# Performance work log

Measured on AMD Instinct MI355X. Metric: run time of the kernel, lower is better.

Reference implementation:

```python
import jax, jax.numpy as jnp
import numpy as np

EMBED_DIM = 1024
NUM_HEADS = 16
HEAD_DIM = EMBED_DIM // NUM_HEADS


def setup_inputs() -> dict:
    key = jax.random.key(0)
    ks = jax.random.split(key, 5)
    s = 0.02
    return {
        "x": jax.random.normal(ks[0], (2, 2048, EMBED_DIM), dtype=jnp.float32),
        "w_qkv": jax.random.normal(ks[1], (EMBED_DIM, 3 * EMBED_DIM), dtype=jnp.float32) * s,
        "b_qkv": jnp.zeros((3 * EMBED_DIM,), dtype=jnp.float32),
        "w_out": jax.random.normal(ks[2], (EMBED_DIM, EMBED_DIM), dtype=jnp.float32) * s,
        "b_out": jnp.zeros((EMBED_DIM,), dtype=jnp.float32),
    }


def reference(x, w_qkv, b_qkv, w_out, b_out):
    B, T, C = x.shape
    qkv = x @ w_qkv + b_qkv                       # [B,T,3C]
    q, k, v = jnp.split(qkv, 3, axis=-1)
    # [B,T,C] -> [B,H,T,Dh]
    def heads(t):
        return t.reshape(B, T, NUM_HEADS, HEAD_DIM).transpose(0, 2, 1, 3)
    q, k, v = heads(q), heads(k), heads(v)
    scale = 1.0 / np.sqrt(HEAD_DIM).astype(np.float32)
    scores = jnp.einsum("bhqd,bhkd->bhqk", q, k) * scale  # [B,H,T,T]
    causal = jnp.tril(jnp.ones((T, T), dtype=bool))
    scores = jnp.where(causal[None, None], scores, -jnp.inf)
    attn = jax.nn.softmax(scores, axis=-1)
    out = jnp.einsum("bhqk,bhkd->bhqd", attn, v)  # [B,H,T,Dh]
    out = out.transpose(0, 2, 1, 3).reshape(B, T, C)
    return out @ w_out + b_out
```

## Files before the change

### kernel.cpp

```cpp
#include <hip/hip_runtime.h>

typedef unsigned short u16;
typedef unsigned int u32;
typedef __attribute__((ext_vector_type(8))) short bf16x8;
typedef __attribute__((ext_vector_type(4))) float f32x4;
typedef __attribute__((ext_vector_type(16))) float f32x16;

#define TOK   4096
#define EMB   1024
#define NQKV  3072
#define TSEQ  2048
#define NH    16

__device__ __forceinline__ u16 f2b(float f) {
  union { float f; unsigned u; } v; v.f = f;
  unsigned r = v.u + 0x7FFFu + ((v.u >> 16) & 1u);
  return (u16)(r >> 16);
}

__device__ __forceinline__ u32 pack_rn(float a, float b) {
  u32 ua = __float_as_uint(a) + 0x8000u;
  u32 ub = __float_as_uint(b) + 0x8000u;
  return __builtin_amdgcn_perm(ub, ua, 0x07060302u);
}

__device__ __forceinline__ f32x16 zero16() {
  f32x16 z;
#pragma unroll
  for (int i = 0; i < 16; i++) z[i] = 0.f;
  return z;
}

__device__ __forceinline__ void gload16(const void* g, void* l) {
  __builtin_amdgcn_global_load_lds((const __attribute__((address_space(1))) void*)g,
                                   (__attribute__((address_space(3))) void*)l, 16, 0, 0);
}


__global__ __launch_bounds__(256) void prep_kernel(const float* __restrict__ x,
                                                   u16* __restrict__ x_bf,
                                                   const float* __restrict__ w_qkv,
                                                   u16* __restrict__ wqkvT,
                                                   const float* __restrict__ w_out,
                                                   u16* __restrict__ woutT) {
  __shared__ u16 sm[64][65];
  int bid = blockIdx.x, tid = threadIdx.x;
  if (bid < 4096) {
    int i = bid * 256 + tid;
    float4 v = ((const float4*)x)[i];
    union { u16 us[4]; uint2 u2; } o;
    o.us[0] = f2b(v.x); o.us[1] = f2b(v.y); o.us[2] = f2b(v.z); o.us[3] = f2b(v.w);
    ((uint2*)x_bf)[i] = o.u2;
    return;
  }
  const float* src; u16* dst; int R, C, bx, by;
  if (bid < 4096 + 768) {
    int t = bid - 4096; bx = t % 48; by = t / 48;
    src = w_qkv; dst = wqkvT; R = EMB; C = NQKV;
  } else {
    int t = bid - 4096 - 768; bx = t & 15; by = t >> 4;
    src = w_out; dst = woutT; R = EMB; C = EMB;
  }
  int c0 = bx * 64, r0 = by * 64;
#pragma unroll
  for (int i = 0; i < 16; i++) {
    int idx = tid + i * 256;
    int r = idx >> 6, c = idx & 63;
    sm[r][c] = f2b(src[(size_t)(r0 + r) * C + c0 + c]);
  }
  __syncthreads();
#pragma unroll
  for (int i = 0; i < 16; i++) {
    int idx = tid + i * 256;
    int cc = idx >> 6, rr = idx & 63;
    dst[(size_t)(c0 + cc) * R + r0 + rr] = sm[rr][cc];
  }
}

__global__ __launch_bounds__(256) void transpose_v(const u16* __restrict__ V,
                                                   u16* __restrict__ Vt) {
  __shared__ u16 sm[64][72];
  int t0 = blockIdx.x * 64, bh = blockIdx.y;
  size_t base = (size_t)bh * TSEQ * 64;
  int tid = threadIdx.x;
  int r = tid >> 2, c = (tid & 3) * 16;
  *(bf16x8*)&sm[r][c]     = *(const bf16x8*)&V[base + (size_t)(t0 + r) * 64 + c];
  *(bf16x8*)&sm[r][c + 8] = *(const bf16x8*)&V[base + (size_t)(t0 + r) * 64 + c + 8];
  __syncthreads();
  int d = tid >> 2, tc = (tid & 3) * 16;
  union { u16 us[16]; uint4 v4[2]; } o;
#pragma unroll
  for (int i = 0; i < 16; i++) o.us[i] = sm[tc + i][d];
  *(uint4*)&Vt[base + (size_t)d * TSEQ + t0 + tc]     = o.v4[0];
  *(uint4*)&Vt[base + (size_t)d * TSEQ + t0 + tc + 8] = o.v4[1];
}


template <int MODE, int TN>
__global__ __launch_bounds__(256) void gemm_bt(const u16* __restrict__ A,
                                               const u16* __restrict__ Bt,
                                               const float* __restrict__ bias,
                                               u16* __restrict__ qb, u16* __restrict__ kb,
                                               u16* __restrict__ vb, float* __restrict__ outp,
                                               int K, int N) {
  constexpr int CT = TN / 32;
  constexpr int RB = TN / 32;
  __shared__ u16 As[2][128][64];
  __shared__ u16 Bs[2][TN][64];
  int tid = threadIdx.x;
  int m0 = blockIdx.y * 128, n0 = blockIdx.x * TN;
  int lane = tid & 63, wid = tid >> 6;
  int wm = (wid >> 1) * 64;
  int wn = (wid & 1) * (TN / 2);
  int l15 = lane & 15, quad = lane >> 4;
  int srow = lane >> 3;
  int scol = (((lane & 7) ^ srow) * 8);

  f32x4 acc[4][CT];
#pragma unroll
  for (int i = 0; i < 4; i++)
#pragma unroll
    for (int j = 0; j < CT; j++) acc[i][j] = (f32x4){0.f, 0.f, 0.f, 0.f};

  const u16* Ag = A + (size_t)(m0 + wid * 32 + srow) * K + scol;
  const u16* Bg = Bt + (size_t)(n0 + wid * (TN / 4) + srow) * K + scol;

#pragma unroll
  for (int i = 0; i < 4; i++)
    gload16(Ag + (size_t)(i * 8) * K, &As[0][wid * 32 + i * 8][0]);
#pragma unroll
  for (int i = 0; i < RB; i++)
    gload16(Bg + (size_t)(i * 8) * K, &Bs[0][wid * (TN / 4) + i * 8][0]);
  __syncthreads();

  int cur = 0;
  for (int k0 = 0; k0 < K; k0 += 64) {
    if (k0 + 64 < K) {
      int kn = k0 + 64;
#pragma unroll
      for (int i = 0; i < 4; i++)
        gload16(Ag + (size_t)(i * 8) * K + kn, &As[cur ^ 1][wid * 32 + i * 8][0]);
#pragma unroll
      for (int i = 0; i < RB; i++)
        gload16(Bg + (size_t)(i * 8) * K + kn, &Bs[cur ^ 1][wid * (TN / 4) + i * 8][0]);
    }

#pragma unroll
    for (int ks = 0; ks < 2; ks++) {
      bf16x8 af[4], bfr[CT];
#pragma unroll
      for (int rt = 0; rt < 4; rt++)
        af[rt] = *(const bf16x8*)&As[cur][wm + rt * 16 + l15][((ks * 4 + quad) ^ (l15 & 7)) * 8];
#pragma unroll
      for (int ct = 0; ct < CT; ct++)
        bfr[ct] = *(const bf16x8*)&Bs[cur][wn + ct * 16 + l15][((ks * 4 + quad) ^ (l15 & 7)) * 8];
#pragma unroll
      for (int rt = 0; rt < 4; rt++)
#pragma unroll
        for (int ct = 0; ct < CT; ct++)
          acc[rt][ct] = __builtin_amdgcn_mfma_f32_16x16x32_bf16(bfr[ct], af[rt], acc[rt][ct], 0, 0, 0);
    }
    __syncthreads();
    cur ^= 1;
  }

#pragma unroll
  for (int rt = 0; rt < 4; rt++) {
#pragma unroll
    for (int ct = 0; ct < CT; ct++) {
      int m = m0 + wm + rt * 16 + l15;
      int nb = n0 + wn + ct * 16 + quad * 4;
      float4 b4 = *(const float4*)&bias[nb];
      float v0 = acc[rt][ct][0] + b4.x, v1 = acc[rt][ct][1] + b4.y;
      float v2 = acc[rt][ct][2] + b4.z, v3 = acc[rt][ct][3] + b4.w;
      if (MODE == 0) {
        int sel = nb >> 10;
        int c = nb & 1023;
        int h = c >> 6, d0 = c & 63;
        int b = m >> 11, t = m & 2047;
        u16* dst = (sel == 0) ? qb : (sel == 1) ? kb : vb;
        union { u32 u[2]; uint2 u2; } o;
        o.u[0] = pack_rn(v0, v1);
        o.u[1] = pack_rn(v2, v3);
        *(uint2*)&dst[((((size_t)b * NH + h) * TSEQ + t) << 6) + d0] = o.u2;
      } else {
        float4 o = {v0, v1, v2, v3};
        *(float4*)&outp[(size_t)m * N + nb] = o;
      }
    }
  }
}


__global__ __launch_bounds__(256, 4) void attn_kernel(const u16* __restrict__ Qb,
                                                      const u16* __restrict__ Kb,
                                                      const u16* __restrict__ Vtb,
                                                      u16* __restrict__ O) {
  __shared__ u16 Ks[64][68];
  __shared__ u16 Vt[64][68];
  __shared__ float Cmb[2][16][64][2];
  __shared__ float Lmb[2][32];

  const float SCL = 0.18033688f;
  const float MOFF = 16.0f;

  int phys = blockIdx.x;
  int xcd = phys & 7;
  int cuL = (phys >> 3) & 31;
  int slot = phys >> 8;
  int bh = xcd * 4 + slot;
  int qt = (slot & 1) ? (31 - cuL) : cuL;

  int tid = threadIdx.x, lane = tid & 63, w = tid >> 6;
  int sub = w & 1, par = w >> 1;
  int l31 = lane & 31, h = lane >> 5;
  const size_t hoff = (size_t)bh * TSEQ * 64;

  int qw = qt * 64 + sub * 32;
  int qg = qw + l31;

  bf16x8 qf[4];
  {
    const u16* qp = Qb + hoff + (size_t)qg * 64 + h * 8;
#pragma unroll
    for (int s = 0; s < 4; s++) qf[s] = *(const bf16x8*)(qp + s * 16);
  }

  f32x16 acc[2];
  acc[0] = zero16(); acc[1] = zero16();
  float l_i = 0.f;

  int r = tid >> 2, cb = (tid & 3) * 16;
  bf16x8 kr0, kr1, vr0, vr1;
  {
    const u16* kg = Kb + hoff + (size_t)r * 64 + cb;
    const u16* vg = Vtb + hoff + (size_t)r * TSEQ + cb;
    kr0 = *(const bf16x8*)kg;       kr1 = *(const bf16x8*)(kg + 8);
    vr0 = *(const bf16x8*)vg;       vr1 = *(const bf16x8*)(vg + 8);
  }

  for (int kt = 0; kt <= qt; kt++) {
    __syncthreads();
    *(bf16x8*)&Ks[r][cb]     = kr0;
    *(bf16x8*)&Ks[r][cb + 8] = kr1;
    *(bf16x8*)&Vt[r][cb]     = vr0;
    *(bf16x8*)&Vt[r][cb + 8] = vr1;
    __syncthreads();
    if (kt < qt) {
      const u16* kg = Kb + hoff + (size_t)((kt + 1) * 64 + r) * 64 + cb;
      const u16* vg = Vtb + hoff + (size_t)r * TSEQ + (kt + 1) * 64 + cb;
      kr0 = *(const bf16x8*)kg;     kr1 = *(const bf16x8*)(kg + 8);
      vr0 = *(const bf16x8*)vg;     vr1 = *(const bf16x8*)(vg + 8);
    }

    int kbt = kt * 64 + par * 32;
    if (kbt <= qw + 31) {
      f32x16 sacc = zero16();
#pragma unroll
      for (int s = 0; s < 4; s++) {
        bf16x8 kf = *(const bf16x8*)&Ks[par * 32 + l31][s * 16 + h * 8];
        sacc = __builtin_amdgcn_mfma_f32_32x32x16_bf16(kf, qf[s], sacc, 0, 0, 0);
      }

      if (kbt + 31 > qw) {
#pragma unroll
        for (int rr = 0; rr < 16; rr++) {
          int key = kbt + (rr & 3) + 8 * (rr >> 2) + 4 * h;
          if (key > qg) sacc[rr] = -1e30f;
        }
      }

#pragma unroll
      for (int rr = 0; rr < 16; rr++) {
        float p = exp2f(__builtin_fmaf(sacc[rr], SCL, -MOFF));
        sacc[rr] = p;
        l_i += p;
      }

#pragma unroll
      for (int s2 = 0; s2 < 2; s2++) {
        u32 u0 = pack_rn(sacc[8 * s2 + 0], sacc[8 * s2 + 1]);
        u32 u1 = pack_rn(sacc[8 * s2 + 2], sacc[8 * s2 + 3]);
        u32 u2 = pack_rn(sacc[8 * s2 + 4], sacc[8 * s2 + 5]);
        u32 u3 = pack_rn(sacc[8 * s2 + 6], sacc[8 * s2 + 7]);
        u32 s0 = h ? u0 : u2, s1 = h ? u1 : u3;
        u32 t0 = (u32)__shfl_xor((int)s0, 32);
        u32 t1 = (u32)__shfl_xor((int)s1, 32);
        union { u32 d[4]; bf16x8 v; } pf;
        pf.d[0] = h ? t0 : u0;
        pf.d[1] = h ? t1 : u1;
        pf.d[2] = h ? u2 : t0;
        pf.d[3] = h ? u3 : t1;
#pragma unroll
        for (int dt = 0; dt < 2; dt++) {
          bf16x8 vf = *(const bf16x8*)&Vt[dt * 32 + l31][par * 32 + s2 * 16 + h * 8];
          acc[dt] = __builtin_amdgcn_mfma_f32_32x32x16_bf16(vf, pf.v, acc[dt], 0, 0, 0);
        }
      }
    }
  }

  l_i += __shfl_xor(l_i, 32);

  __syncthreads();
  if (par == 1) {
#pragma unroll
    for (int dt = 0; dt < 2; dt++)
#pragma unroll
      for (int pr = 0; pr < 8; pr++) {
        Cmb[sub][dt * 8 + pr][lane][0] = acc[dt][2 * pr];
        Cmb[sub][dt * 8 + pr][lane][1] = acc[dt][2 * pr + 1];
      }
    if (h == 0) Lmb[sub][l31] = l_i;
  }
  __syncthreads();
  if (par == 0) {
#pragma unroll
    for (int dt = 0; dt < 2; dt++)
#pragma unroll
      for (int pr = 0; pr < 8; pr++) {
        acc[dt][2 * pr]     += Cmb[sub][dt * 8 + pr][lane][0];
        acc[dt][2 * pr + 1] += Cmb[sub][dt * 8 + pr][lane][1];
      }
    float lt = l_i + Lmb[sub][l31];
    float inv = 1.0f / lt;

    int b = bh >> 4, head = bh & 15;
    size_t rowbase = ((size_t)b * TSEQ + qg) * 1024 + head * 64;
#pragma unroll
    for (int dt = 0; dt < 2; dt++)
#pragma unroll
      for (int G = 0; G < 4; G++) {
        union { u32 u[2]; uint2 u2; } o;
        o.u[0] = pack_rn(acc[dt][4 * G + 0] * inv, acc[dt][4 * G + 1] * inv);
        o.u[1] = pack_rn(acc[dt][4 * G + 2] * inv, acc[dt][4 * G + 3] * inv);
        *(uint2*)&O[rowbase + dt * 32 + G * 8 + 4 * h] = o.u2;
      }
  }
}


extern "C" void kernel_launch(void* const* d_in, const int* in_sizes, int n_in,
                              void* d_out, int out_size, void* d_ws, size_t ws_size,
                              hipStream_t stream) {
  (void)in_sizes; (void)n_in; (void)out_size; (void)ws_size;
  const float* x     = (const float*)d_in[0];
  const float* w_qkv = (const float*)d_in[1];
  const float* b_qkv = (const float*)d_in[2];
  const float* w_out = (const float*)d_in[3];
  const float* b_out = (const float*)d_in[4];
  float* out = (float*)d_out;

  char* p = (char*)d_ws;
  u16* x_bf  = (u16*)p; p += (size_t)TOK * EMB * 2;
  u16* wqkvT = (u16*)p; p += (size_t)NQKV * EMB * 2;
  u16* woutT = (u16*)p; p += (size_t)EMB * EMB * 2;
  u16* Qb    = (u16*)p; p += (size_t)32 * TSEQ * 64 * 2;
  u16* Kb    = (u16*)p; p += (size_t)32 * TSEQ * 64 * 2;
  u16* Vraw  = (u16*)p; p += (size_t)32 * TSEQ * 64 * 2;
  u16* attn_o = (u16*)p;
  u16* Vtb   = x_bf;

  prep_kernel<<<dim3(4096 + 768 + 256), 256, 0, stream>>>(x, x_bf, w_qkv, wqkvT, w_out, woutT);
  gemm_bt<0, 128><<<dim3(NQKV / 128, TOK / 128), 256, 0, stream>>>(x_bf, wqkvT, b_qkv,
                                                                   Qb, Kb, Vraw, nullptr, EMB, NQKV);
  transpose_v<<<dim3(TSEQ / 64, 32), 256, 0, stream>>>(Vraw, Vtb);
  attn_kernel<<<dim3(1024), 256, 0, stream>>>(Qb, Kb, Vtb, attn_o);
  gemm_bt<1, 64><<<dim3(EMB / 64, TOK / 128), 256, 0, stream>>>(attn_o, woutT, b_out,
                                                                nullptr, nullptr, nullptr, out, EMB, EMB);
}
```

Baseline: 195.6 us.

## Fuse V transpose into QKV GEMM epilogue, vectorize weight transpose, use permlane32 swap

The V transpose kernel is removed: the QKV GEMM epilogue now writes V directly in d-major (transposed) layout with scalar 2-byte stores. The weight-transpose part of the prep kernel now writes 16-element vectorized rows instead of scalar stores. In attention, the manual bf16 packing plus two cross-half shuffles is replaced by the hardware v_cvt_pk_bf16_f32 instruction and permlane32_swap. The scattered scalar V stores in the GEMM epilogue are strided by TSEQ and may be uncoalesced, which could offset the saved launch and round trip.

New measurement: 182.9 us. -6.5%, faster.

```diff
diff --git a/kernel.cpp b/kernel.cpp
--- a/kernel.cpp
+++ b/kernel.cpp
@@ -2,6 +2,7 @@
 
 typedef unsigned short u16;
 typedef unsigned int u32;
+typedef __attribute__((ext_vector_type(2))) unsigned int u32x2;
 typedef __attribute__((ext_vector_type(8))) short bf16x8;
 typedef __attribute__((ext_vector_type(4))) float f32x4;
 typedef __attribute__((ext_vector_type(16))) float f32x16;
@@ -16,6 +17,10 @@
   union { float f; unsigned u; } v; v.f = f;
   unsigned r = v.u + 0x7FFFu + ((v.u >> 16) & 1u);
   return (u16)(r >> 16);
+}
+
+__device__ __forceinline__ u16 f2b_hu(float f) {
+  return (u16)((__float_as_uint(f) + 0x8000u) >> 16);
 }
 
 __device__ __forceinline__ u32 pack_rn(float a, float b) {
@@ -69,30 +74,12 @@
     sm[r][c] = f2b(src[(size_t)(r0 + r) * C + c0 + c]);
   }
   __syncthreads();
-#pragma unroll
-  for (int i = 0; i < 16; i++) {
-    int idx = tid + i * 256;
-    int cc = idx >> 6, rr = idx & 63;
-    dst[(size_t)(c0 + cc) * R + r0 + rr] = sm[rr][cc];
-  }
-}
-
-__global__ __launch_bounds__(256) void transpose_v(const u16* __restrict__ V,
-                                                   u16* __restrict__ Vt) {
-  __shared__ u16 sm[64][72];
-  int t0 = blockIdx.x * 64, bh = blockIdx.y;
-  size_t base = (size_t)bh * TSEQ * 64;
-  int tid = threadIdx.x;
-  int r = tid >> 2, c = (tid & 3) * 16;
-  *(bf16x8*)&sm[r][c]     = *(const bf16x8*)&V[base + (size_t)(t0 + r) * 64 + c];
-  *(bf16x8*)&sm[r][c + 8] = *(const bf16x8*)&V[base + (size_t)(t0 + r) * 64 + c + 8];
-  __syncthreads();
-  int d = tid >> 2, tc = (tid & 3) * 16;
+  int cc2 = tid >> 2, rr0 = (tid & 3) * 16;
   union { u16 us[16]; uint4 v4[2]; } o;
 #pragma unroll
-  for (int i = 0; i < 16; i++) o.us[i] = sm[tc + i][d];
-  *(uint4*)&Vt[base + (size_t)d * TSEQ + t0 + tc]     = o.v4[0];
-  *(uint4*)&Vt[base + (size_t)d * TSEQ + t0 + tc + 8] = o.v4[1];
+  for (int j = 0; j < 16; j++) o.us[j] = sm[rr0 + j][cc2];
+  *(uint4*)&dst[(size_t)(c0 + cc2) * R + r0 + rr0]     = o.v4[0];
+  *(uint4*)&dst[(size_t)(c0 + cc2) * R + r0 + rr0 + 8] = o.v4[1];
 }
 
 
@@ -178,11 +165,19 @@
         int c = nb & 1023;
         int h = c >> 6, d0 = c & 63;
         int b = m >> 11, t = m & 2047;
-        u16* dst = (sel == 0) ? qb : (sel == 1) ? kb : vb;
-        union { u32 u[2]; uint2 u2; } o;
-        o.u[0] = pack_rn(v0, v1);
-        o.u[1] = pack_rn(v2, v3);
-        *(uint2*)&dst[((((size_t)b * NH + h) * TSEQ + t) << 6) + d0] = o.u2;
+        if (sel == 2) {
+          size_t vbase = ((((size_t)b * NH + h) * 64 + d0) * TSEQ) + t;
+          vb[vbase]            = f2b_hu(v0);
+          vb[vbase + TSEQ]     = f2b_hu(v1);
+          vb[vbase + 2 * TSEQ] = f2b_hu(v2);
+          vb[vbase + 3 * TSEQ] = f2b_hu(v3);
+        } else {
+          u16* dst = sel ? kb : qb;
+          union { u32 u[2]; uint2 u2; } o;
+          o.u[0] = pack_rn(v0, v1);
+          o.u[1] = pack_rn(v2, v3);
+          *(uint2*)&dst[((((size_t)b * NH + h) * TSEQ + t) << 6) + d0] = o.u2;
+        }
       } else {
         float4 o = {v0, v1, v2, v3};
         *(float4*)&outp[(size_t)m * N + nb] = o;
@@ -279,18 +274,18 @@
 
 #pragma unroll
       for (int s2 = 0; s2 < 2; s2++) {
-        u32 u0 = pack_rn(sacc[8 * s2 + 0], sacc[8 * s2 + 1]);
-        u32 u1 = pack_rn(sacc[8 * s2 + 2], sacc[8 * s2 + 3]);
-        u32 u2 = pack_rn(sacc[8 * s2 + 4], sacc[8 * s2 + 5]);
-        u32 u3 = pack_rn(sacc[8 * s2 + 6], sacc[8 * s2 + 7]);
-        u32 s0 = h ? u0 : u2, s1 = h ? u1 : u3;
-        u32 t0 = (u32)__shfl_xor((int)s0, 32);
-        u32 t1 = (u32)__shfl_xor((int)s1, 32);
+        u32 u0, u1, u2, u3;
+        asm("v_cvt_pk_bf16_f32 %0, %1, %2" : "=v"(u0) : "v"(sacc[8 * s2 + 0]), "v"(sacc[8 * s2 + 1]));
+        asm("v_cvt_pk_bf16_f32 %0, %1, %2" : "=v"(u1) : "v"(sacc[8 * s2 + 2]), "v"(sacc[8 * s2 + 3]));
+        asm("v_cvt_pk_bf16_f32 %0, %1, %2" : "=v"(u2) : "v"(sacc[8 * s2 + 4]), "v"(sacc[8 * s2 + 5]));
+        asm("v_cvt_pk_bf16_f32 %0, %1, %2" : "=v"(u3) : "v"(sacc[8 * s2 + 6]), "v"(sacc[8 * s2 + 7]));
+        u32x2 r02 = __builtin_amdgcn_permlane32_swap(u0, u2, false, false);
+        u32x2 r13 = __builtin_amdgcn_permlane32_swap(u1, u3, false, false);
         union { u32 d[4]; bf16x8 v; } pf;
-        pf.d[0] = h ? t0 : u0;
-        pf.d[1] = h ? t1 : u1;
-        pf.d[2] = h ? u2 : t0;
-        pf.d[3] = h ? u3 : t1;
+        pf.d[0] = r02[0];
+        pf.d[1] = r13[0];
+        pf.d[2] = r02[1];
+        pf.d[3] = r13[1];
 #pragma unroll
         for (int dt = 0; dt < 2; dt++) {
           bf16x8 vf = *(const bf16x8*)&Vt[dt * 32 + l31][par * 32 + s2 * 16 + h * 8];
@@ -357,14 +352,12 @@
   u16* woutT = (u16*)p; p += (size_t)EMB * EMB * 2;
   u16* Qb    = (u16*)p; p += (size_t)32 * TSEQ * 64 * 2;
   u16* Kb    = (u16*)p; p += (size_t)32 * TSEQ * 64 * 2;
-  u16* Vraw  = (u16*)p; p += (size_t)32 * TSEQ * 64 * 2;
+  u16* Vtb   = (u16*)p; p += (size_t)32 * TSEQ * 64 * 2;
   u16* attn_o = (u16*)p;
-  u16* Vtb   = x_bf;
 
   prep_kernel<<<dim3(4096 + 768 + 256), 256, 0, stream>>>(x, x_bf, w_qkv, wqkvT, w_out, woutT);
   gemm_bt<0, 128><<<dim3(NQKV / 128, TOK / 128), 256, 0, stream>>>(x_bf, wqkvT, b_qkv,
-                                                                   Qb, Kb, Vraw, nullptr, EMB, NQKV);
-  transpose_v<<<dim3(TSEQ / 64, 32), 256, 0, stream>>>(Vraw, Vtb);
+                                                                   Qb, Kb, Vtb, nullptr, EMB, NQKV);
   attn_kernel<<<dim3(1024), 256, 0, stream>>>(Qb, Kb, Vtb, attn_o);
   gemm_bt<1, 64><<<dim3(EMB / 64, TOK / 128), 256, 0, stream>>>(attn_o, woutT, b_out,
                                                                 nullptr, nullptr, nullptr, out, EMB, EMB);
```
